# Kernel optimization log

Hardware: AMD Instinct MI355X
Metric: run time of the kernel (lower is better)

Reference implementation:

```python
import jax, jax.numpy as jnp
import numpy as np

E, T, D, H = 4, 4096, 2048, 8192

def setup_inputs() -> dict:
    key = jax.random.key(0)
    k1, k2, k3 = jax.random.split(key, 3)
    x = jax.random.normal(k1, (E, T, D), dtype=jnp.float32)
    fc1_w = jax.random.normal(k2, (E, D, H), dtype=jnp.float32) * 0.001
    fc2_w = jax.random.normal(k3, (E, H, D), dtype=jnp.float32) * 0.001
    fc1_b = jnp.zeros((E, 1, H), dtype=jnp.float32)
    fc2_b = jnp.zeros((E, 1, D), dtype=jnp.float32)
    return {"x": x, "fc1_w": fc1_w, "fc1_b": fc1_b, "fc2_w": fc2_w, "fc2_b": fc2_b}

def reference(x, fc1_w, fc1_b, fc2_w, fc2_b):
    # batched expert FFN: y = relu(x @ W1 + b1) @ W2 + b2, per expert e
    y = jnp.einsum('etd,edh->eth', x, fc1_w) + fc1_b
    y = jax.nn.relu(y)
    y = jnp.einsum('eth,ehd->etd', y, fc2_w) + fc2_b
    return y
```

## Files before the change

kernel.cpp:

```cpp
#include <hip/hip_runtime.h>
#include <hip/hip_bf16.h>
#include <stdint.h>

#define E_ 4
#define T_ 4096
#define D_ 2048
#define H_ 8192

typedef __attribute__((ext_vector_type(8))) short bf16x8;
typedef __attribute__((ext_vector_type(4))) float f32x4;
typedef __attribute__((ext_vector_type(4))) unsigned short u16x4;

__device__ __forceinline__ unsigned short f2bf(float f) {
    unsigned int u = __float_as_uint(f);
    u = u + 0x7fffu + ((u >> 16) & 1u);
    return (unsigned short)(u >> 16);
}

__device__ __forceinline__ void async16(const unsigned short* g, unsigned short* l) {
    auto gp = (const __attribute__((address_space(1))) unsigned int*)g;
    auto lp = (__attribute__((address_space(3))) unsigned int*)l;
    __builtin_amdgcn_global_load_lds(gp, lp, 16 , 0 , 0 );
}

__device__ __forceinline__ f32x4 mfma16(bf16x8 a, bf16x8 b, f32x4 c) {
    return __builtin_amdgcn_mfma_f32_16x16x32_bf16(a, b, c, 0, 0, 0);
}

__global__ void cvt_x_kernel(const float4* __restrict__ in, uint2* __restrict__ out, long n4) {
    long i = (long)blockIdx.x * blockDim.x + threadIdx.x;
    long stride = (long)gridDim.x * blockDim.x;
    for (; i < n4; i += stride) {
        float4 v = in[i];
        uint2 o;
        o.x = (unsigned)f2bf(v.x) | ((unsigned)f2bf(v.y) << 16);
        o.y = (unsigned)f2bf(v.z) | ((unsigned)f2bf(v.w) << 16);
        out[i] = o;
    }
}

__global__ void transpose_cvt_kernel(const float* __restrict__ W, unsigned short* __restrict__ Wt,
                                     int R, int C) {
    __shared__ float tile[64][65];
    const float* Wp = W + (size_t)blockIdx.z * R * C;
    unsigned short* Wtp = Wt + (size_t)blockIdx.z * R * C;
    const int c0 = blockIdx.x * 64, r0 = blockIdx.y * 64;
    const int tc = threadIdx.x & 63;
    const int tr = threadIdx.x >> 6;
#pragma unroll
    for (int i = 0; i < 16; ++i) {
        int r = tr * 16 + i;
        tile[r][tc] = Wp[(size_t)(r0 + r) * C + c0 + tc];
    }
    __syncthreads();
#pragma unroll
    for (int i = 0; i < 16; ++i) {
        int r = tr * 16 + i;
        Wtp[(size_t)(c0 + r) * R + r0 + tc] = f2bf(tile[tc][r]);
    }
}

template <int K, int OUT_MODE>
__global__ __launch_bounds__(512, 2) void gemm256_kernel(
    const unsigned short* __restrict__ A,
    const unsigned short* __restrict__ Bt,
    const float* __restrict__ bias,
    void* __restrict__ Cout,
    int M, int N)
{
    constexpr int BK = 64;
    constexpr int NT = K / BK;
    __shared__ __align__(16) unsigned short L[2][2][2][128][64];

    const int nx = gridDim.x, ny = gridDim.y;
    const int nwg = nx * ny * gridDim.z;
    const int w = (blockIdx.z * ny + blockIdx.y) * nx + blockIdx.x;
    const int cpx = nwg >> 3;
    const int xcd = w & 7;
    const int c = w >> 3;
    const int CR = cpx / nx;
    const int GX = (nx % 16 == 0) ? 16 : nx;
    const int g = c / (GX * CR);
    const int r1 = c - g * (GX * CR);
    const int byl = r1 / GX;
    const int bxi = r1 - byl * GX;
    const int fy = xcd * CR + byl;
    const int bx = g * GX + bxi;
    const int e = fy / ny;
    const int by = fy - e * ny;

    const unsigned short* Ae = A + (size_t)e * M * K;
    const unsigned short* Be = Bt + (size_t)e * N * K;
    const int bm0 = by * 256;
    const int bn0 = bx * 256;

    const int tid = threadIdx.x;
    const int lane = tid & 63;
    const int wid = tid >> 6;
    const int wr = wid >> 2;
    const int wc = wid & 3;

    const int srow = wid * 16 + (lane >> 3);
    const int skel = 8 * ((lane & 7) ^ (lane >> 3));

    const int fr = lane & 15;
    const int kq = lane >> 4;
    const int ksw = (lane & 7) << 3;
    const int bh = wc >> 1;
    const int brb = (wc & 1) * 64;

    f32x4 acc[8][4] = {};

    auto stageA = [&](int t, int h) {
        const int k0 = t * BK;
        const int s = t & 1;
#pragma unroll
        for (int i = 0; i < 2; ++i) {
            async16(Ae + (size_t)(bm0 + h * 128 + srow + i * 8) * K + k0 + skel,
                    &L[s][0][h][wid * 16 + i * 8][0]);
        }
    };
    auto stageB = [&](int t, int h) {
        const int k0 = t * BK;
        const int s = t & 1;
#pragma unroll
        for (int i = 0; i < 2; ++i) {
            async16(Be + (size_t)(bn0 + h * 128 + srow + i * 8) * K + k0 + skel,
                    &L[s][1][h][wid * 16 + i * 8][0]);
        }
    };

    stageB(0, 0); stageB(0, 1); stageA(0, 0); stageA(0, 1);
    stageB(1, 0); stageB(1, 1); stageA(1, 0); stageA(1, 1);

    bf16x8 a[4][2], b[4][2];

    for (int t = 0; t < NT; ++t) {
        const int s = t & 1;

        if (t == NT - 1) {
            asm volatile("s_waitcnt vmcnt(0)" ::: "memory");
        } else {
            asm volatile("s_waitcnt vmcnt(8)" ::: "memory");
        }
        __builtin_amdgcn_s_barrier();

#pragma unroll
        for (int n = 0; n < 2; ++n)
#pragma unroll
            for (int kk = 0; kk < 2; ++kk)
                b[n][kk] = *(const bf16x8*)&L[s][1][bh][brb + n * 16 + fr][(kk * 32 + kq * 8) ^ ksw];
#pragma unroll
        for (int m = 0; m < 4; ++m)
#pragma unroll
            for (int kk = 0; kk < 2; ++kk)
                a[m][kk] = *(const bf16x8*)&L[s][0][wr][m * 16 + fr][(kk * 32 + kq * 8) ^ ksw];
#pragma unroll
        for (int n = 2; n < 4; ++n)
#pragma unroll
            for (int kk = 0; kk < 2; ++kk)
                b[n][kk] = *(const bf16x8*)&L[s][1][bh][brb + n * 16 + fr][(kk * 32 + kq * 8) ^ ksw];

        __builtin_amdgcn_s_setprio(1);
#pragma unroll
        for (int m = 0; m < 4; ++m)
#pragma unroll
            for (int n = 0; n < 4; ++n)
#pragma unroll
                for (int kk = 0; kk < 2; ++kk)
                    acc[m][n] = mfma16(a[m][kk], b[n][kk], acc[m][n]);
        __builtin_amdgcn_s_setprio(0);

#pragma unroll
        for (int m = 0; m < 4; ++m)
#pragma unroll
            for (int kk = 0; kk < 2; ++kk)
                a[m][kk] = *(const bf16x8*)&L[s][0][wr][(m + 4) * 16 + fr][(kk * 32 + kq * 8) ^ ksw];

        asm volatile("s_waitcnt lgkmcnt(0)" ::: "memory");
        __builtin_amdgcn_sched_barrier(0);
        __builtin_amdgcn_s_barrier();

        if (t + 2 < NT) {
            stageB(t + 2, 0); stageB(t + 2, 1);
            stageA(t + 2, 0); stageA(t + 2, 1);
        }
        __builtin_amdgcn_sched_barrier(0);

        __builtin_amdgcn_s_setprio(1);
#pragma unroll
        for (int m = 0; m < 4; ++m)
#pragma unroll
            for (int n = 0; n < 4; ++n)
#pragma unroll
                for (int kk = 0; kk < 2; ++kk)
                    acc[m + 4][n] = mfma16(a[m][kk], b[n][kk], acc[m + 4][n]);
        __builtin_amdgcn_s_setprio(0);
    }

    constexpr int ST = 260;
    float* S = (float*)&L[0][0][0][0][0];
    const int rowq = (lane >> 4) * 4;
    const float* bp = bias + (size_t)e * N;
    const float4 bb4 = *(const float4*)(bp + bn0 + lane * 4);

    unsigned short* Y = (unsigned short*)Cout + (size_t)e * M * N;
    float* O = (float*)Cout + (size_t)e * M * N;

#pragma unroll
    for (int s = 0; s < 8; ++s) {
        __syncthreads();
        if (wr == (s >> 2)) {
            const int sl = s & 3;
#pragma unroll
            for (int mm = 0; mm < 2; ++mm) {
#pragma unroll
                for (int n = 0; n < 4; ++n) {
#pragma unroll
                    for (int j = 0; j < 4; ++j) {
                        S[(mm * 16 + rowq + j) * ST + wc * 64 + n * 16 + fr] =
                            acc[2 * sl + mm][n][j];
                    }
                }
            }
        }
        __syncthreads();
#pragma unroll
        for (int rr = 0; rr < 4; ++rr) {
            const int rl = wid * 4 + rr;
            const int rg = bm0 + s * 32 + rl;
            f32x4 v = *(const f32x4*)&S[rl * ST + lane * 4];
            v[0] += bb4.x; v[1] += bb4.y; v[2] += bb4.z; v[3] += bb4.w;
            if (OUT_MODE == 0) {
                u16x4 o;
                o[0] = f2bf(fmaxf(v[0], 0.0f));
                o[1] = f2bf(fmaxf(v[1], 0.0f));
                o[2] = f2bf(fmaxf(v[2], 0.0f));
                o[3] = f2bf(fmaxf(v[3], 0.0f));
                *(u16x4*)(Y + (size_t)rg * N + bn0 + lane * 4) = o;
            } else {
                *(f32x4*)(O + (size_t)rg * N + bn0 + lane * 4) = v;
            }
        }
    }
}

extern "C" void kernel_launch(void* const* d_in, const int* in_sizes, int n_in,
                              void* d_out, int out_size, void* d_ws, size_t ws_size,
                              hipStream_t stream) {
    const float* x     = (const float*)d_in[0];
    const float* fc1_w = (const float*)d_in[1];
    const float* fc1_b = (const float*)d_in[2];
    const float* fc2_w = (const float*)d_in[3];
    const float* fc2_b = (const float*)d_in[4];
    float* out = (float*)d_out;

    const size_t n_x  = (size_t)E_ * T_ * D_;
    const size_t n_w1 = (size_t)E_ * D_ * H_;
    const size_t n_w2 = (size_t)E_ * H_ * D_;
    const size_t n_y1 = (size_t)E_ * T_ * H_;

    const size_t need = (n_x + n_w1 + n_w2 + n_y1) * sizeof(unsigned short);
    if (ws_size < need) return;

    unsigned short* xb  = (unsigned short*)d_ws;
    unsigned short* w1t = xb + n_x;
    unsigned short* w2t = w1t + n_w1;
    unsigned short* y1  = w2t + n_w2;

    cvt_x_kernel<<<2048, 256, 0, stream>>>((const float4*)x, (uint2*)xb, (long)(n_x / 4));
    {
        dim3 g(H_ / 64, D_ / 64, E_);
        transpose_cvt_kernel<<<g, 256, 0, stream>>>(fc1_w, w1t, D_, H_);
    }
    {
        dim3 g(D_ / 64, H_ / 64, E_);
        transpose_cvt_kernel<<<g, 256, 0, stream>>>(fc2_w, w2t, H_, D_);
    }
    {
        dim3 g(H_ / 256, T_ / 256, E_);
        gemm256_kernel<D_, 0><<<g, 512, 0, stream>>>(xb, w1t, fc1_b, (void*)y1, T_, H_);
    }
    {
        dim3 g(D_ / 256, T_ / 256, E_);
        gemm256_kernel<H_, 1><<<g, 512, 0, stream>>>(y1, w2t, fc2_b, (void*)out, T_, D_);
    }
}
```

Measured before the change: 1.160 ms.

## Switch GEMM inner loop to 32x32x16 MFMA with precomputed LDS pointers

Replaces the 16x16x32 bf16 MFMA tiles with 32x32x16 MFMA, reorganizing per-wave fragments into 4x2 blocks of 32x32 accumulators and remapping the LDS read pattern and epilogue scatter to match. Global load addresses become incrementing pointers instead of recomputed offsets, and the k-loop is manually unrolled by two so stage indices are compile-time constants. The aim is fewer MFMA and LDS-read instructions per FLOP and less address arithmetic, at the cost of a new swizzle/fragment mapping that must match the staging layout exactly.

```diff
diff --git a/kernel.cpp b/kernel.cpp
--- a/kernel.cpp
+++ b/kernel.cpp
@@ -9,6 +9,7 @@
 
 typedef __attribute__((ext_vector_type(8))) short bf16x8;
 typedef __attribute__((ext_vector_type(4))) float f32x4;
+typedef __attribute__((ext_vector_type(16))) float f32x16;
 typedef __attribute__((ext_vector_type(4))) unsigned short u16x4;
 
 __device__ __forceinline__ unsigned short f2bf(float f) {
@@ -23,8 +24,8 @@
     __builtin_amdgcn_global_load_lds(gp, lp, 16 , 0 , 0 );
 }
 
-__device__ __forceinline__ f32x4 mfma16(bf16x8 a, bf16x8 b, f32x4 c) {
-    return __builtin_amdgcn_mfma_f32_16x16x32_bf16(a, b, c, 0, 0, 0);
+__device__ __forceinline__ f32x16 mfma32(bf16x8 a, bf16x8 b, f32x16 c) {
+    return __builtin_amdgcn_mfma_f32_32x32x16_bf16(a, b, c, 0, 0, 0);
 }
 
 __global__ void cvt_x_kernel(const float4* __restrict__ in, uint2* __restrict__ out, long n4) {
@@ -103,124 +104,129 @@
     const int srow = wid * 16 + (lane >> 3);
     const int skel = 8 * ((lane & 7) ^ (lane >> 3));
 
-    const int fr = lane & 15;
-    const int kq = lane >> 4;
-    const int ksw = (lane & 7) << 3;
-    const int bh = wc >> 1;
-    const int brb = (wc & 1) * 64;
-
-    f32x4 acc[8][4] = {};
-
-    auto stageA = [&](int t, int h) {
-        const int k0 = t * BK;
-        const int s = t & 1;
-#pragma unroll
-        for (int i = 0; i < 2; ++i) {
-            async16(Ae + (size_t)(bm0 + h * 128 + srow + i * 8) * K + k0 + skel,
-                    &L[s][0][h][wid * 16 + i * 8][0]);
-        }
-    };
-    auto stageB = [&](int t, int h) {
-        const int k0 = t * BK;
-        const int s = t & 1;
-#pragma unroll
-        for (int i = 0; i < 2; ++i) {
-            async16(Be + (size_t)(bn0 + h * 128 + srow + i * 8) * K + k0 + skel,
-                    &L[s][1][h][wid * 16 + i * 8][0]);
-        }
-    };
-
-    stageB(0, 0); stageB(0, 1); stageA(0, 0); stageA(0, 1);
-    stageB(1, 0); stageB(1, 1); stageA(1, 0); stageA(1, 1);
-
-    bf16x8 a[4][2], b[4][2];
-
-    for (int t = 0; t < NT; ++t) {
-        const int s = t & 1;
-
-        if (t == NT - 1) {
-            asm volatile("s_waitcnt vmcnt(0)" ::: "memory");
-        } else {
-            asm volatile("s_waitcnt vmcnt(8)" ::: "memory");
-        }
-        __builtin_amdgcn_s_barrier();
-
-#pragma unroll
-        for (int n = 0; n < 2; ++n)
-#pragma unroll
-            for (int kk = 0; kk < 2; ++kk)
-                b[n][kk] = *(const bf16x8*)&L[s][1][bh][brb + n * 16 + fr][(kk * 32 + kq * 8) ^ ksw];
-#pragma unroll
-        for (int m = 0; m < 4; ++m)
-#pragma unroll
-            for (int kk = 0; kk < 2; ++kk)
-                a[m][kk] = *(const bf16x8*)&L[s][0][wr][m * 16 + fr][(kk * 32 + kq * 8) ^ ksw];
-#pragma unroll
-        for (int n = 2; n < 4; ++n)
-#pragma unroll
-            for (int kk = 0; kk < 2; ++kk)
-                b[n][kk] = *(const bf16x8*)&L[s][1][bh][brb + n * 16 + fr][(kk * 32 + kq * 8) ^ ksw];
-
-        __builtin_amdgcn_s_setprio(1);
-#pragma unroll
-        for (int m = 0; m < 4; ++m)
-#pragma unroll
-            for (int n = 0; n < 4; ++n)
-#pragma unroll
-                for (int kk = 0; kk < 2; ++kk)
-                    acc[m][n] = mfma16(a[m][kk], b[n][kk], acc[m][n]);
-        __builtin_amdgcn_s_setprio(0);
-
-#pragma unroll
-        for (int m = 0; m < 4; ++m)
-#pragma unroll
-            for (int kk = 0; kk < 2; ++kk)
-                a[m][kk] = *(const bf16x8*)&L[s][0][wr][(m + 4) * 16 + fr][(kk * 32 + kq * 8) ^ ksw];
-
-        asm volatile("s_waitcnt lgkmcnt(0)" ::: "memory");
-        __builtin_amdgcn_sched_barrier(0);
-        __builtin_amdgcn_s_barrier();
-
-        if (t + 2 < NT) {
-            stageB(t + 2, 0); stageB(t + 2, 1);
-            stageA(t + 2, 0); stageA(t + 2, 1);
-        }
-        __builtin_amdgcn_sched_barrier(0);
-
-        __builtin_amdgcn_s_setprio(1);
-#pragma unroll
-        for (int m = 0; m < 4; ++m)
-#pragma unroll
-            for (int n = 0; n < 4; ++n)
-#pragma unroll
-                for (int kk = 0; kk < 2; ++kk)
-                    acc[m + 4][n] = mfma16(a[m][kk], b[n][kk], acc[m + 4][n]);
-        __builtin_amdgcn_s_setprio(0);
-    }
+    const unsigned short* gA00 = Ae + (size_t)(bm0 +   0 + srow + 0) * K + skel;
+    const unsigned short* gA01 = Ae + (size_t)(bm0 +   0 + srow + 8) * K + skel;
+    const unsigned short* gA10 = Ae + (size_t)(bm0 + 128 + srow + 0) * K + skel;
+    const unsigned short* gA11 = Ae + (size_t)(bm0 + 128 + srow + 8) * K + skel;
+    const unsigned short* gB00 = Be + (size_t)(bn0 +   0 + srow + 0) * K + skel;
+    const unsigned short* gB01 = Be + (size_t)(bn0 +   0 + srow + 8) * K + skel;
+    const unsigned short* gB10 = Be + (size_t)(bn0 + 128 + srow + 0) * K + skel;
+    const unsigned short* gB11 = Be + (size_t)(bn0 + 128 + srow + 8) * K + skel;
+
+#define STAGE_ALL(S_) do {                                   \
+        async16(gB00, &L[S_][1][0][wid * 16 + 0][0]);        \
+        async16(gB01, &L[S_][1][0][wid * 16 + 8][0]);        \
+        async16(gB10, &L[S_][1][1][wid * 16 + 0][0]);        \
+        async16(gB11, &L[S_][1][1][wid * 16 + 8][0]);        \
+        async16(gA00, &L[S_][0][0][wid * 16 + 0][0]);        \
+        async16(gA01, &L[S_][0][0][wid * 16 + 8][0]);        \
+        async16(gA10, &L[S_][0][1][wid * 16 + 0][0]);        \
+        async16(gA11, &L[S_][0][1][wid * 16 + 8][0]);        \
+    } while (0)
+
+#define BUMP_ALL() do {                                      \
+        gA00 += BK; gA01 += BK; gA10 += BK; gA11 += BK;      \
+        gB00 += BK; gB01 += BK; gB10 += BK; gB11 += BK;      \
+    } while (0)
+
+    const int r5 = lane & 31;
+    const int kh = lane >> 5;
+    const int q  = lane & 7;
+    const int g0e = 8 * (kh ^ q);
+    const unsigned short* Lp = &L[0][0][0][0][0];
+    const unsigned short* pk[2][4];
+#pragma unroll
+    for (int s = 0; s < 2; ++s)
+#pragma unroll
+        for (int ks = 0; ks < 4; ++ks)
+            pk[s][ks] = Lp + s * 32768 + r5 * 64 + (g0e ^ (ks * 16));
+
+    const int AOFF = wr * 8192;
+    const int BOFF = 16384 + (wc >> 1) * 8192 + (wc & 1) * 4096;
+
+    f32x16 acc[4][2] = {};
+
+    STAGE_ALL(0);
+    BUMP_ALL();
+    STAGE_ALL(1);
+    BUMP_ALL();
+
+    bf16x8 a[2][4], b[2][4];
+
+#define BODY(T_, S_) do {                                                              \
+        if ((T_) == NT - 1) asm volatile("s_waitcnt vmcnt(0)" ::: "memory");           \
+        else                asm volatile("s_waitcnt vmcnt(8)" ::: "memory");           \
+        __builtin_amdgcn_s_barrier();                                                  \
+        _Pragma("unroll")                                                              \
+        for (int nb = 0; nb < 2; ++nb)                                                 \
+            _Pragma("unroll")                                                          \
+            for (int ks = 0; ks < 4; ++ks)                                             \
+                b[nb][ks] = *(const bf16x8*)(pk[S_][ks] + BOFF + nb * 2048);           \
+        _Pragma("unroll")                                                              \
+        for (int mb = 0; mb < 2; ++mb)                                                 \
+            _Pragma("unroll")                                                          \
+            for (int ks = 0; ks < 4; ++ks)                                             \
+                a[mb][ks] = *(const bf16x8*)(pk[S_][ks] + AOFF + mb * 2048);           \
+        __builtin_amdgcn_s_setprio(1);                                                 \
+        _Pragma("unroll")                                                              \
+        for (int mb = 0; mb < 2; ++mb)                                                 \
+            _Pragma("unroll")                                                          \
+            for (int nb = 0; nb < 2; ++nb)                                             \
+                _Pragma("unroll")                                                      \
+                for (int ks = 0; ks < 4; ++ks)                                         \
+                    acc[mb][nb] = mfma32(a[mb][ks], b[nb][ks], acc[mb][nb]);           \
+        __builtin_amdgcn_s_setprio(0);                                                 \
+        _Pragma("unroll")                                                              \
+        for (int mb = 0; mb < 2; ++mb)                                                 \
+            _Pragma("unroll")                                                          \
+            for (int ks = 0; ks < 4; ++ks)                                             \
+                a[mb][ks] = *(const bf16x8*)(pk[S_][ks] + AOFF + (mb + 2) * 2048);     \
+        asm volatile("s_waitcnt lgkmcnt(0)" ::: "memory");                             \
+        __builtin_amdgcn_sched_barrier(0);                                             \
+        __builtin_amdgcn_s_barrier();                                                  \
+        if ((T_) + 2 < NT) { STAGE_ALL(S_); }                                          \
+        __builtin_amdgcn_sched_barrier(0);                                             \
+        __builtin_amdgcn_s_setprio(1);                                                 \
+        _Pragma("unroll")                                                              \
+        for (int mb = 0; mb < 2; ++mb)                                                 \
+            _Pragma("unroll")                                                          \
+            for (int nb = 0; nb < 2; ++nb)                                             \
+                _Pragma("unroll")                                                      \
+                for (int ks = 0; ks < 4; ++ks)                                         \
+                    acc[mb + 2][nb] = mfma32(a[mb][ks], b[nb][ks], acc[mb + 2][nb]);   \
+        __builtin_amdgcn_s_setprio(0);                                                 \
+        BUMP_ALL();                                                                    \
+    } while (0)
+
+    for (int t = 0; t < NT; t += 2) {
+        BODY(t, 0);
+        BODY(t + 1, 1);
+    }
+#undef BODY
+#undef STAGE_ALL
+#undef BUMP_ALL
 
     constexpr int ST = 260;
     float* S = (float*)&L[0][0][0][0][0];
-    const int rowq = (lane >> 4) * 4;
     const float* bp = bias + (size_t)e * N;
     const float4 bb4 = *(const float4*)(bp + bn0 + lane * 4);
+    const int c5 = lane & 31;
+    const int hi = lane >> 5;
 
     unsigned short* Y = (unsigned short*)Cout + (size_t)e * M * N;
     float* O = (float*)Cout + (size_t)e * M * N;
 
 #pragma unroll
-    for (int s = 0; s < 8; ++s) {
+    for (int sg = 0; sg < 8; ++sg) {
         __syncthreads();
-        if (wr == (s >> 2)) {
-            const int sl = s & 3;
-#pragma unroll
-            for (int mm = 0; mm < 2; ++mm) {
-#pragma unroll
-                for (int n = 0; n < 4; ++n) {
-#pragma unroll
-                    for (int j = 0; j < 4; ++j) {
-                        S[(mm * 16 + rowq + j) * ST + wc * 64 + n * 16 + fr] =
-                            acc[2 * sl + mm][n][j];
-                    }
+        if (wr == (sg >> 2)) {
+            const int mb = sg & 3;
+#pragma unroll
+            for (int nb = 0; nb < 2; ++nb) {
+#pragma unroll
+                for (int r = 0; r < 16; ++r) {
+                    const int rf = (r & 3) + 8 * (r >> 2) + 4 * hi;
+                    S[rf * ST + wc * 64 + nb * 32 + c5] = acc[mb][nb][r];
                 }
             }
         }
@@ -228,7 +234,7 @@
 #pragma unroll
         for (int rr = 0; rr < 4; ++rr) {
             const int rl = wid * 4 + rr;
-            const int rg = bm0 + s * 32 + rl;
+            const int rg = bm0 + sg * 32 + rl;
             f32x4 v = *(const f32x4*)&S[rl * ST + lane * 4];
             v[0] += bb4.x; v[1] += bb4.y; v[2] += bb4.z; v[3] += bb4.w;
             if (OUT_MODE == 0) {
```

Result: slower. 1.442 ms (+24.3%).

## Software-pipeline LDS fragment loads for next K-tile behind MFMA of current tile

Applied to the files above, without the earlier changes.

Restructures the GEMM main loop so the A/B fragment reads for tile t+1 are issued from LDS while the second half of tile t's MFMAs runs, with a prologue that preloads tile 0. The global-load wait and barrier move to mid-iteration so the next buffer is ready before its fragments are read. The aim is to hide LDS read latency at the start of each iteration behind matrix work. The cost is more complex wait accounting (vmcnt(0) over the last two iterations) and the risk that the reordering around barriers creates hazards on the double buffer.

```diff
diff --git a/kernel.cpp b/kernel.cpp
--- a/kernel.cpp
+++ b/kernel.cpp
@@ -132,70 +132,99 @@
 
     stageB(0, 0); stageB(0, 1); stageA(0, 0); stageA(0, 1);
     stageB(1, 0); stageB(1, 1); stageA(1, 0); stageA(1, 1);
+    asm volatile("s_waitcnt vmcnt(8)" ::: "memory");
+    __builtin_amdgcn_sched_barrier(0);
+    __builtin_amdgcn_s_barrier();
 
     bf16x8 a[4][2], b[4][2];
+#pragma unroll
+    for (int n = 0; n < 4; ++n)
+#pragma unroll
+        for (int kk = 0; kk < 2; ++kk)
+            b[n][kk] = *(const bf16x8*)&L[0][1][bh][brb + n * 16 + fr][(kk * 32 + kq * 8) ^ ksw];
+#pragma unroll
+    for (int m = 0; m < 4; ++m)
+#pragma unroll
+        for (int kk = 0; kk < 2; ++kk)
+            a[m][kk] = *(const bf16x8*)&L[0][0][wr][m * 16 + fr][(kk * 32 + kq * 8) ^ ksw];
 
     for (int t = 0; t < NT; ++t) {
         const int s = t & 1;
 
-        if (t == NT - 1) {
+        __builtin_amdgcn_s_setprio(1);
+#pragma unroll
+        for (int m = 0; m < 4; ++m)
+#pragma unroll
+            for (int n = 0; n < 4; ++n)
+#pragma unroll
+                for (int kk = 0; kk < 2; ++kk)
+                    acc[m][n] = mfma16(a[m][kk], b[n][kk], acc[m][n]);
+        __builtin_amdgcn_s_setprio(0);
+
+#pragma unroll
+        for (int m = 0; m < 4; ++m)
+#pragma unroll
+            for (int kk = 0; kk < 2; ++kk)
+                a[m][kk] = *(const bf16x8*)&L[s][0][wr][(m + 4) * 16 + fr][(kk * 32 + kq * 8) ^ ksw];
+
+        asm volatile("s_waitcnt lgkmcnt(0)" ::: "memory");
+        __builtin_amdgcn_sched_barrier(0);
+        __builtin_amdgcn_s_barrier();
+
+        if (t + 2 < NT) {
+            stageB(t + 2, 0); stageB(t + 2, 1);
+            stageA(t + 2, 0); stageA(t + 2, 1);
+        }
+        __builtin_amdgcn_sched_barrier(0);
+
+        if (t >= NT - 2) {
             asm volatile("s_waitcnt vmcnt(0)" ::: "memory");
         } else {
             asm volatile("s_waitcnt vmcnt(8)" ::: "memory");
         }
-        __builtin_amdgcn_s_barrier();
-
-#pragma unroll
-        for (int n = 0; n < 2; ++n)
-#pragma unroll
-            for (int kk = 0; kk < 2; ++kk)
-                b[n][kk] = *(const bf16x8*)&L[s][1][bh][brb + n * 16 + fr][(kk * 32 + kq * 8) ^ ksw];
-#pragma unroll
-        for (int m = 0; m < 4; ++m)
-#pragma unroll
-            for (int kk = 0; kk < 2; ++kk)
-                a[m][kk] = *(const bf16x8*)&L[s][0][wr][m * 16 + fr][(kk * 32 + kq * 8) ^ ksw];
-#pragma unroll
-        for (int n = 2; n < 4; ++n)
-#pragma unroll
-            for (int kk = 0; kk < 2; ++kk)
-                b[n][kk] = *(const bf16x8*)&L[s][1][bh][brb + n * 16 + fr][(kk * 32 + kq * 8) ^ ksw];
-
-        __builtin_amdgcn_s_setprio(1);
-#pragma unroll
-        for (int m = 0; m < 4; ++m)
-#pragma unroll
-            for (int n = 0; n < 4; ++n)
-#pragma unroll
-                for (int kk = 0; kk < 2; ++kk)
-                    acc[m][n] = mfma16(a[m][kk], b[n][kk], acc[m][n]);
-        __builtin_amdgcn_s_setprio(0);
-
-#pragma unroll
-        for (int m = 0; m < 4; ++m)
-#pragma unroll
-            for (int kk = 0; kk < 2; ++kk)
-                a[m][kk] = *(const bf16x8*)&L[s][0][wr][(m + 4) * 16 + fr][(kk * 32 + kq * 8) ^ ksw];
-
-        asm volatile("s_waitcnt lgkmcnt(0)" ::: "memory");
         __builtin_amdgcn_sched_barrier(0);
         __builtin_amdgcn_s_barrier();
 
-        if (t + 2 < NT) {
-            stageB(t + 2, 0); stageB(t + 2, 1);
-            stageA(t + 2, 0); stageA(t + 2, 1);
-        }
-        __builtin_amdgcn_sched_barrier(0);
-
         __builtin_amdgcn_s_setprio(1);
 #pragma unroll
         for (int m = 0; m < 4; ++m)
 #pragma unroll
-            for (int n = 0; n < 4; ++n)
+            for (int n = 0; n < 2; ++n)
 #pragma unroll
                 for (int kk = 0; kk < 2; ++kk)
                     acc[m + 4][n] = mfma16(a[m][kk], b[n][kk], acc[m + 4][n]);
         __builtin_amdgcn_s_setprio(0);
+
+        if (t + 1 < NT) {
+#pragma unroll
+            for (int n = 0; n < 2; ++n)
+#pragma unroll
+                for (int kk = 0; kk < 2; ++kk)
+                    b[n][kk] = *(const bf16x8*)&L[s ^ 1][1][bh][brb + n * 16 + fr][(kk * 32 + kq * 8) ^ ksw];
+        }
+
+        __builtin_amdgcn_s_setprio(1);
+#pragma unroll
+        for (int m = 0; m < 4; ++m)
+#pragma unroll
+            for (int n = 2; n < 4; ++n)
+#pragma unroll
+                for (int kk = 0; kk < 2; ++kk)
+                    acc[m + 4][n] = mfma16(a[m][kk], b[n][kk], acc[m + 4][n]);
+        __builtin_amdgcn_s_setprio(0);
+
+        if (t + 1 < NT) {
+#pragma unroll
+            for (int n = 2; n < 4; ++n)
+#pragma unroll
+                for (int kk = 0; kk < 2; ++kk)
+                    b[n][kk] = *(const bf16x8*)&L[s ^ 1][1][bh][brb + n * 16 + fr][(kk * 32 + kq * 8) ^ ksw];
+#pragma unroll
+            for (int m = 0; m < 4; ++m)
+#pragma unroll
+                for (int kk = 0; kk < 2; ++kk)
+                    a[m][kk] = *(const bf16x8*)&L[s ^ 1][0][wr][m * 16 + fr][(kk * 32 + kq * 8) ^ ksw];
+        }
     }
 
     constexpr int ST = 260;
@@ -208,10 +237,10 @@
     float* O = (float*)Cout + (size_t)e * M * N;
 
 #pragma unroll
-    for (int s = 0; s < 8; ++s) {
+    for (int sg = 0; sg < 8; ++sg) {
         __syncthreads();
-        if (wr == (s >> 2)) {
-            const int sl = s & 3;
+        if (wr == (sg >> 2)) {
+            const int sl = sg & 3;
 #pragma unroll
             for (int mm = 0; mm < 2; ++mm) {
 #pragma unroll
@@ -228,7 +257,7 @@
 #pragma unroll
         for (int rr = 0; rr < 4; ++rr) {
             const int rl = wid * 4 + rr;
-            const int rg = bm0 + s * 32 + rl;
+            const int rg = bm0 + sg * 32 + rl;
             f32x4 v = *(const f32x4*)&S[rl * ST + lane * 4];
             v[0] += bb4.x; v[1] += bb4.y; v[2] += bb4.z; v[3] += bb4.w;
             if (OUT_MODE == 0) {
```

Result: slower. 1.215 ms (+4.8%).
